# Kernel optimization log

Hardware: AMD Instinct MI355X
Metric: run time of the kernel (lower is better)

Reference implementation:

```python
import jax, jax.numpy as jnp
import numpy as np

KH, KW = 3, 3
STRIDE, PAD, DIL = 1, 1, 1


def _unfold(x, kh, kw, stride, pad, dil):
    # torch.nn.functional.unfold equivalent: [B,C,H,W] -> [B, C*kh*kw, L]
    # conv_general_dilated_patches flattens feature dim in (C, kh, kw) order,
    # which matches torch unfold's channel-major ordering.
    p = jax.lax.conv_general_dilated_patches(
        x,
        filter_shape=(kh, kw),
        window_strides=(stride, stride),
        padding=[(pad, pad), (pad, pad)],
        rhs_dilation=(dil, dil),
    )  # [B, C*kh*kw, Ho, Wo]
    b, ck, ho, wo = p.shape
    return p.reshape(b, ck, ho * wo)


def setup_inputs() -> dict:
    key = jax.random.key(0)
    k1, k2, k3 = jax.random.split(key, 3)
    B, C, H, W_sp = 4, 8, 128, 128
    N, K = 8, KH * KW
    array = jax.random.normal(k1, (B, C, H, W_sp), dtype=jnp.float32)
    W = jax.random.normal(k2, (N, C, K, 1), dtype=jnp.float32)
    Bbias = jax.random.normal(k3, (N, C, 1, 1), dtype=jnp.float32)
    return {"array": array, "W": W, "Bbias": Bbias}


def reference(array, W, Bbias):
    Bn, C, H, W_sp = array.shape
    N, _, K, _ = W.shape
    # unfold -> [B, 1, C, K, L]  (matches torch reshape + unsqueeze(1))
    patches = _unfold(array, KH, KW, STRIDE, PAD, DIL).reshape(Bn, 1, C, K, -1)
    L = patches.shape[-1]
    mul = patches * W[None]                         # [B, N, C, K, L]
    size = jnp.sum(W, axis=2, keepdims=True)        # [N, C, 1, 1] (sum over K)
    mean = jnp.mean(mul, axis=3, keepdims=True)     # [B, N, C, 1, L]
    i = (mul - mean) ** 2 / size + Bbias[None]      # weighted variance + bias
    return i.reshape(Bn, -1, L)                     # [B, N*C*K, L]
```

## Files before the change

### kernel.cpp

```cpp
#include <hip/hip_runtime.h>


#define BB 4
#define NN 8
#define CC 8
#define KK 9
#define HH 128
#define WW 128
#define LL (HH * WW)

typedef float vf4 __attribute__((ext_vector_type(4)));

__global__ __launch_bounds__(256) void tvar_kernel(
    const float* __restrict__ arr,
    const float* __restrict__ Wt,
    const float* __restrict__ Bb,
    float* __restrict__ out)
{
    const int tid = blockIdx.x * blockDim.x + threadIdx.x;
    const int w4 = tid & 31;
    const int h  = (tid >> 5) & 127;
    const int c  = (tid >> 12) & 7;
    const int b  = tid >> 15;

    __shared__ float sW[NN][KK];
    __shared__ float sInv[NN];
    __shared__ float sBias[NN];
    const int lt = threadIdx.x;
    if (lt < NN * KK) {
        const int n = lt / KK, k = lt - n * KK;
        sW[n][k] = Wt[(n * CC + c) * KK + k];
    }
    __syncthreads();
    if (lt < NN) {
        float s = 0.f;
        #pragma unroll
        for (int k = 0; k < KK; ++k) s += sW[lt][k];
        sInv[lt]  = 1.0f / s;
        sBias[lt] = Bb[lt * CC + c];
    }
    __syncthreads();

    const int ws = w4 << 2;
    const float* abase = arr + (size_t)((b * CC + c) * HH) * WW;
    float p[3][6];
    #pragma unroll
    for (int r = 0; r < 3; ++r) {
        const int hh = h + r - 1;
        if (hh >= 0 && hh < HH) {
            const float* row = abase + hh * WW + ws;
            const float4 v = *(const float4*)row;
            p[r][1] = v.x; p[r][2] = v.y; p[r][3] = v.z; p[r][4] = v.w;
            p[r][0] = (ws > 0)       ? row[-1] : 0.f;
            p[r][5] = (ws + 4 < WW)  ? row[4]  : 0.f;
        } else {
            #pragma unroll
            for (int j = 0; j < 6; ++j) p[r][j] = 0.f;
        }
    }

    float* obase = out + (size_t)b * (NN * CC * KK) * LL + (size_t)(h * WW + ws);
    const float inv9 = 1.0f / 9.0f;

    #pragma unroll
    for (int n = 0; n < NN; ++n) {
        float w9[KK];
        #pragma unroll
        for (int k = 0; k < KK; ++k) w9[k] = sW[n][k];
        const float sinv = sInv[n];
        const float bias = sBias[n];

        float mean[4] = {0.f, 0.f, 0.f, 0.f};
        #pragma unroll
        for (int k = 0; k < KK; ++k) {
            const int kh = k / 3, kw = k - kh * 3;
            #pragma unroll
            for (int j = 0; j < 4; ++j)
                mean[j] += p[kh][j + kw] * w9[k];
        }
        #pragma unroll
        for (int j = 0; j < 4; ++j) mean[j] *= inv9;

        float* onb = obase + (size_t)((n * CC + c) * KK) * LL;
        #pragma unroll
        for (int k = 0; k < KK; ++k) {
            const int kh = k / 3, kw = k - kh * 3;
            vf4 o;
            #pragma unroll
            for (int j = 0; j < 4; ++j) {
                const float v = p[kh][j + kw] * w9[k];
                const float d = v - mean[j];
                o[j] = d * d * sinv + bias;
            }
            __builtin_nontemporal_store(o, (vf4*)(onb + (size_t)k * LL));
        }
    }
}

extern "C" void kernel_launch(void* const* d_in, const int* in_sizes, int n_in,
                              void* d_out, int out_size, void* d_ws, size_t ws_size,
                              hipStream_t stream) {
    const float* arr = (const float*)d_in[0];
    const float* Wt  = (const float*)d_in[1];
    const float* Bb  = (const float*)d_in[2];
    float* out = (float*)d_out;

    const int threads = 256;
    const int blocks = (BB * CC * HH * (WW / 4)) / threads;
    tvar_kernel<<<blocks, threads, 0, stream>>>(arr, Wt, Bb, out);
}
```

Measured before the change: 158.0 us.

## Parallelize over output channel n per block, drop shared-memory weight staging

Each block now handles a single (b, n, c, 8-row) slice instead of looping over all 8 n values per thread, giving 8x more blocks with less work each. Weights and the bias are read directly into registers per thread, which removes the shared-memory staging and both __syncthreads barriers. The cost is that each input tile is reloaded 8 times (once per n), mostly from cache. The kernel is dominated by output writes, so any gain would come from more parallelism and memory-level concurrency.

```diff
diff --git a/kernel.cpp b/kernel.cpp
--- a/kernel.cpp
+++ b/kernel.cpp
@@ -17,29 +17,23 @@
     const float* __restrict__ Bb,
     float* __restrict__ out)
 {
-    const int tid = blockIdx.x * blockDim.x + threadIdx.x;
-    const int w4 = tid & 31;
-    const int h  = (tid >> 5) & 127;
-    const int c  = (tid >> 12) & 7;
-    const int b  = tid >> 15;
+    const int bid = blockIdx.x;
+    const int hi = bid & 15;
+    const int c  = (bid >> 4) & 7;
+    const int n  = (bid >> 7) & 7;
+    const int b  = bid >> 10;
 
-    __shared__ float sW[NN][KK];
-    __shared__ float sInv[NN];
-    __shared__ float sBias[NN];
     const int lt = threadIdx.x;
-    if (lt < NN * KK) {
-        const int n = lt / KK, k = lt - n * KK;
-        sW[n][k] = Wt[(n * CC + c) * KK + k];
-    }
-    __syncthreads();
-    if (lt < NN) {
-        float s = 0.f;
-        #pragma unroll
-        for (int k = 0; k < KK; ++k) s += sW[lt][k];
-        sInv[lt]  = 1.0f / s;
-        sBias[lt] = Bb[lt * CC + c];
-    }
-    __syncthreads();
+    const int w4 = lt & 31;
+    const int h  = (hi << 3) | (lt >> 5);
+
+    const float* wrow = Wt + (n * CC + c) * KK;
+    float w9[KK];
+    float wsum = 0.f;
+    #pragma unroll
+    for (int k = 0; k < KK; ++k) { w9[k] = wrow[k]; wsum += w9[k]; }
+    const float sinv = 1.0f / wsum;
+    const float bias = Bb[n * CC + c];
 
     const int ws = w4 << 2;
     const float* abase = arr + (size_t)((b * CC + c) * HH) * WW;
@@ -51,49 +45,40 @@
             const float* row = abase + hh * WW + ws;
             const float4 v = *(const float4*)row;
             p[r][1] = v.x; p[r][2] = v.y; p[r][3] = v.z; p[r][4] = v.w;
-            p[r][0] = (ws > 0)       ? row[-1] : 0.f;
-            p[r][5] = (ws + 4 < WW)  ? row[4]  : 0.f;
+            p[r][0] = (ws > 0)      ? row[-1] : 0.f;
+            p[r][5] = (ws + 4 < WW) ? row[4]  : 0.f;
         } else {
             #pragma unroll
             for (int j = 0; j < 6; ++j) p[r][j] = 0.f;
         }
     }
 
-    float* obase = out + (size_t)b * (NN * CC * KK) * LL + (size_t)(h * WW + ws);
     const float inv9 = 1.0f / 9.0f;
+    float mean[4] = {0.f, 0.f, 0.f, 0.f};
+    #pragma unroll
+    for (int k = 0; k < KK; ++k) {
+        const int kh = k / 3, kw = k - kh * 3;
+        #pragma unroll
+        for (int j = 0; j < 4; ++j)
+            mean[j] += p[kh][j + kw] * w9[k];
+    }
+    #pragma unroll
+    for (int j = 0; j < 4; ++j) mean[j] *= inv9;
 
+    float* onb = out + (size_t)b * (NN * CC * KK) * LL
+                     + (size_t)((n * CC + c) * KK) * LL
+                     + (size_t)(h * WW + ws);
     #pragma unroll
-    for (int n = 0; n < NN; ++n) {
-        float w9[KK];
+    for (int k = 0; k < KK; ++k) {
+        const int kh = k / 3, kw = k - kh * 3;
+        vf4 o;
         #pragma unroll
-        for (int k = 0; k < KK; ++k) w9[k] = sW[n][k];
-        const float sinv = sInv[n];
-        const float bias = sBias[n];
-
-        float mean[4] = {0.f, 0.f, 0.f, 0.f};
-        #pragma unroll
-        for (int k = 0; k < KK; ++k) {
-            const int kh = k / 3, kw = k - kh * 3;
-            #pragma unroll
-            for (int j = 0; j < 4; ++j)
-                mean[j] += p[kh][j + kw] * w9[k];
+        for (int j = 0; j < 4; ++j) {
+            const float v = p[kh][j + kw] * w9[k];
+            const float d = v - mean[j];
+            o[j] = d * d * sinv + bias;
         }
-        #pragma unroll
-        for (int j = 0; j < 4; ++j) mean[j] *= inv9;
-
-        float* onb = obase + (size_t)((n * CC + c) * KK) * LL;
-        #pragma unroll
-        for (int k = 0; k < KK; ++k) {
-            const int kh = k / 3, kw = k - kh * 3;
-            vf4 o;
-            #pragma unroll
-            for (int j = 0; j < 4; ++j) {
-                const float v = p[kh][j + kw] * w9[k];
-                const float d = v - mean[j];
-                o[j] = d * d * sinv + bias;
-            }
-            __builtin_nontemporal_store(o, (vf4*)(onb + (size_t)k * LL));
-        }
+        __builtin_nontemporal_store(o, (vf4*)(onb + (size_t)k * LL));
     }
 }
 
@@ -106,6 +91,6 @@
     float* out = (float*)d_out;
 
     const int threads = 256;
-    const int blocks = (BB * CC * HH * (WW / 4)) / threads;
+    const int blocks = BB * NN * CC * 16;
     tvar_kernel<<<blocks, threads, 0, stream>>>(arr, Wt, Bb, out);
 }
```

Measured after the change: 158.2 us. No clear change (+0.2%).
